# Performance work log

Measured on AMD Instinct MI355X. Metric: run time of the kernel, lower is better.

Reference implementation:

```python
import jax, jax.numpy as jnp
import numpy as np

N_NODES = 50000
N_EDGES = 800000
IN_F = 128
HEADS = 8
HEAD_DIM = 16
ALPHA = 0.2  # LeakyReLU negative slope
EPS = 1e-6


def setup_inputs() -> dict:
    key = jax.random.key(0)
    k1, k2, k3, k4 = jax.random.split(key, 4)
    x = jax.random.normal(k1, (N_NODES, IN_F), dtype=jnp.float32)
    edge_index = jax.random.randint(k2, (2, N_EDGES), 0, N_NODES, dtype=jnp.int32)
    std = 1.0 / np.sqrt(IN_F)
    W = jax.random.uniform(k3, (HEADS, IN_F, HEAD_DIM), minval=-std, maxval=std, dtype=jnp.float32)
    a = jax.random.uniform(k4, (HEADS, 2 * HEAD_DIM, 1), minval=-std, maxval=std, dtype=jnp.float32)
    bias = jnp.zeros((HEADS * HEAD_DIM,), dtype=jnp.float32)
    return {"x": x, "edge_index": edge_index, "W": W, "a": a, "bias": bias}


def reference(x, edge_index, W, a, bias):
    N = x.shape[0]
    src = edge_index[0]
    tgt = edge_index[1]
    # per-head linear transform: [N, H, D]
    h = jnp.einsum('nf,hfd->nhd', x, W)
    # split attention vector: a = [a_src; a_tgt], each [H, D]
    a_src = a[:, :HEAD_DIM, 0]
    a_tgt = a[:, HEAD_DIM:, 0]
    # node-level partial scores, then gather (equivalent to concat@a on edges)
    s_node_src = jnp.einsum('nhd,hd->nh', h, a_src)  # [N, H]
    s_node_tgt = jnp.einsum('nhd,hd->nh', h, a_tgt)  # [N, H]
    scores = s_node_src[src] + s_node_tgt[tgt]       # [E, H]
    scores = jnp.where(scores >= 0, scores, ALPHA * scores)  # LeakyReLU
    # edge softmax per target node, per head (global max subtract + clamp, as in source)
    max_per_head = jnp.max(scores, axis=0, keepdims=True)    # [1, H]
    exp_scores = jnp.exp(jnp.clip(scores - max_per_head, -20.0, 20.0))  # [E, H]
    denom = jax.ops.segment_sum(exp_scores, tgt, num_segments=N) + EPS  # [N, H]
    attn = exp_scores / denom[tgt]                                      # [E, H]
    # weighted scatter-add aggregation
    weighted = h[src] * attn[:, :, None]                                # [E, H, D]
    agg = jax.ops.segment_sum(weighted, tgt, num_segments=N)            # [N, H, D]
    out = agg.reshape(N, HEADS * HEAD_DIM) + bias
    return out
```

## Files before the change

### kernel.cpp

```cpp
#include <hip/hip_runtime.h>
#include <stdint.h>

#define N_NODES 50000
#define N_EDGES 800000
#define IN_F 128
#define HEADS 8
#define HEAD_DIM 16
#define ALPHA 0.2f
#define EPSV 1e-6f

#define NB 196
#define CAP 4800

typedef short short8 __attribute__((ext_vector_type(8)));
typedef float floatx4 __attribute__((ext_vector_type(4)));

__device__ __forceinline__ float bf2f(unsigned v) {
    return __uint_as_float(v << 16);
}
__device__ __forceinline__ float bflo(unsigned v) {
    return __uint_as_float(v << 16);
}
__device__ __forceinline__ float bfhi(unsigned v) {
    return __uint_as_float(v & 0xffff0000u);
}
__device__ __forceinline__ unsigned f2bf(float f) {
    unsigned u = __float_as_uint(f);
    return (u + 0x7fffu + ((u >> 16) & 1u)) >> 16;
}

__global__ __launch_bounds__(256) void k_wt(const float* __restrict__ W,
                                            ushort* __restrict__ WTb,
                                            int* __restrict__ gcnt) {
    int i = blockIdx.x * 256 + threadIdx.x;
    int c = i >> 7, f = i & 127;
    WTb[i] = (ushort)f2bf(W[(c >> 4) * 2048 + f * 16 + (c & 15)]);
    if (i < NB) gcnt[i] = 0;
}

__global__ __launch_bounds__(256) void k1_mfma(const float* __restrict__ x,
                                               const ushort* __restrict__ WTb,
                                               const float* __restrict__ a,
                                               ushort* __restrict__ hb,
                                               float* __restrict__ s_src,
                                               float* __restrict__ s_tgt) {
    int t = threadIdx.x;
    int wave = t >> 6, lane = t & 63;
    int quad = lane >> 4, col = lane & 15;
    int nb = blockIdx.x * 64 + wave * 16;

    int na = nb + col;
    int nac = na < N_NODES ? na : (N_NODES - 1);
    const float* xrow = x + (size_t)nac * 128 + quad * 8;

    floatx4 acc[8];
    floatx4 z = {0.f, 0.f, 0.f, 0.f};
#pragma unroll
    for (int ct = 0; ct < 8; ct++) acc[ct] = z;

#pragma unroll
    for (int kc = 0; kc < 4; kc++) {
        float4 f0 = *(const float4*)(xrow + kc * 32);
        float4 f1 = *(const float4*)(xrow + kc * 32 + 4);
        short8 af;
        af[0] = (short)f2bf(f0.x); af[1] = (short)f2bf(f0.y);
        af[2] = (short)f2bf(f0.z); af[3] = (short)f2bf(f0.w);
        af[4] = (short)f2bf(f1.x); af[5] = (short)f2bf(f1.y);
        af[6] = (short)f2bf(f1.z); af[7] = (short)f2bf(f1.w);
#pragma unroll
        for (int ct = 0; ct < 8; ct++) {
            const ushort* wrow = WTb + (size_t)(ct * 16 + col) * 128 + kc * 32 + quad * 8;
            short8 bf = *(const short8*)wrow;
            acc[ct] = __builtin_amdgcn_mfma_f32_16x16x32_bf16(af, bf, acc[ct], 0, 0, 0);
        }
    }

    float af_s[8], af_t[8];
#pragma unroll
    for (int ct = 0; ct < 8; ct++) {
        af_s[ct] = a[ct * 32 + col];
        af_t[ct] = a[ct * 32 + 16 + col];
    }

#pragma unroll
    for (int r = 0; r < 4; r++) {
        int node = nb + quad * 4 + r;
        bool nv = (node < N_NODES);
        if (nv) {
            ushort* hrow = hb + (size_t)node * 128 + col;
#pragma unroll
            for (int ct = 0; ct < 8; ct++)
                hrow[ct * 16] = (ushort)f2bf(acc[ct][r]);
        }
        float ps[8], pt[8];
#pragma unroll
        for (int ct = 0; ct < 8; ct++) {
            float hs = acc[ct][r];
            float vs = hs * af_s[ct];
            float vt = hs * af_t[ct];
#pragma unroll
            for (int off = 1; off < 16; off <<= 1) {
                vs += __shfl_xor(vs, off, 64);
                vt += __shfl_xor(vt, off, 64);
            }
            ps[ct] = vs; pt[ct] = vt;
        }
        if (nv && col == 0) {
            *(float4*)(s_src + (size_t)node * 8)     = make_float4(ps[0], ps[1], ps[2], ps[3]);
            *(float4*)(s_src + (size_t)node * 8 + 4) = make_float4(ps[4], ps[5], ps[6], ps[7]);
            *(float4*)(s_tgt + (size_t)node * 8)     = make_float4(pt[0], pt[1], pt[2], pt[3]);
            *(float4*)(s_tgt + (size_t)node * 8 + 4) = make_float4(pt[4], pt[5], pt[6], pt[7]);
        }
    }
}

__global__ __launch_bounds__(256) void k_passA(const int* __restrict__ srcA,
                                               const int* __restrict__ tgtA,
                                               int* __restrict__ gcnt,
                                               unsigned* __restrict__ bucketbuf) {
    __shared__ int lcnt[NB];
    __shared__ int lbase[NB];
    int t = threadIdx.x;
    if (t < NB) lcnt[t] = 0;
    __syncthreads();

    int base = blockIdx.x * 2048 + t;
    int tg[8], sr[8];
    bool vld[8];
#pragma unroll
    for (int k = 0; k < 8; k++) {
        int e = base + k * 256;
        vld[k] = (e < N_EDGES);
        int ee = vld[k] ? e : 0;
        tg[k] = tgtA[ee];
        sr[k] = srcA[ee];
    }
#pragma unroll
    for (int k = 0; k < 8; k++)
        if (vld[k]) atomicAdd(&lcnt[tg[k] >> 8], 1);
    __syncthreads();
    if (t < NB) {
        int c = lcnt[t];
        lbase[t] = (c > 0) ? atomicAdd(&gcnt[t], c) : 0;
        lcnt[t] = 0;
    }
    __syncthreads();
#pragma unroll
    for (int k = 0; k < 8; k++) {
        if (vld[k]) {
            int b = tg[k] >> 8;
            int off = atomicAdd(&lcnt[b], 1);
            int pos = lbase[b] + off;
            if (pos < CAP)
                bucketbuf[(size_t)b * CAP + pos] =
                    ((unsigned)(tg[k] & 255) << 16) | (unsigned)sr[k];
        }
    }
}

__global__ __launch_bounds__(256) void k_passB(const unsigned* __restrict__ bucketbuf,
                                               const int* __restrict__ gcnt,
                                               int* __restrict__ rowptr,
                                               ushort* __restrict__ src16) {
    __shared__ int bin[256];
    __shared__ int wsum[4];
    __shared__ int woff[4];
    __shared__ int sbase;
    __shared__ ushort stage[CAP];
    int t = threadIdx.x, lane = t & 63, w = t >> 6;
    int b = blockIdx.x;

    bin[t] = 0;
    int g = (t < NB) ? gcnt[t] : 0;
    int incg = g;
#pragma unroll
    for (int off = 1; off < 64; off <<= 1) {
        int nn = __shfl_up(incg, off, 64);
        if (lane >= off) incg += nn;
    }
    if (lane == 63) wsum[w] = incg;
    __syncthreads();
    if (t == 0) {
        woff[0] = 0;
        woff[1] = wsum[0];
        woff[2] = wsum[0] + wsum[1];
        woff[3] = wsum[0] + wsum[1] + wsum[2];
    }
    __syncthreads();
    if (t == b) sbase = woff[w] + incg - g;
    if (b == 0 && t == 0) rowptr[N_NODES] = N_EDGES;
    __syncthreads();
    int base = sbase;
    int n = gcnt[b]; if (n > CAP) n = CAP;
    const unsigned* buf = bucketbuf + (size_t)b * CAP;

    for (int i = t; i < n; i += 256)
        atomicAdd(&bin[buf[i] >> 16], 1);
    __syncthreads();
    int v = bin[t];
    int inc = v;
#pragma unroll
    for (int off = 1; off < 64; off <<= 1) {
        int nn = __shfl_up(inc, off, 64);
        if (lane >= off) inc += nn;
    }
    if (lane == 63) wsum[w] = inc;
    __syncthreads();
    if (t == 0) {
        woff[0] = 0;
        woff[1] = wsum[0];
        woff[2] = wsum[0] + wsum[1];
        woff[3] = wsum[0] + wsum[1] + wsum[2];
    }
    __syncthreads();
    int excl = woff[w] + inc - v;
    int node = b * 256 + t;
    if (node < N_NODES) rowptr[node] = base + excl;
    __syncthreads();
    bin[t] = excl;
    __syncthreads();
    for (int i = t; i < n; i += 256) {
        unsigned p = buf[i];
        int off = atomicAdd(&bin[p >> 16], 1);
        stage[off] = (ushort)(p & 0xffffu);
    }
    __syncthreads();
    for (int i = t; i < n; i += 256)
        src16[base + i] = stage[i];
}

__global__ __launch_bounds__(256) void k_fused(const int* __restrict__ rowptr,
                                               const ushort* __restrict__ src16,
                                               const float* __restrict__ s_src,
                                               const float* __restrict__ s_tgt,
                                               const unsigned* __restrict__ h16,
                                               const float* __restrict__ bias,
                                               float* __restrict__ outb) {
    int t = threadIdx.x;
    int wave = t >> 6, lane = t & 63;
    int half = lane >> 5, hl = lane & 31;
    int n = blockIdx.x * 8 + wave * 2 + half;
    int head = hl >> 2;
    int c = 4 * hl;

    const uint2* h2 = (const uint2*)h16;

    float st = s_tgt[n * 8 + head];
    int begin = rowptr[n], end = rowptr[n + 1];

    float ax = 0.f, ay = 0.f, az = 0.f, aw = 0.f, den = 0.f;
    int e = begin;
    for (; e + 3 < end; e += 4) {
        int s0 = src16[e];
        int s1 = src16[e + 1];
        int s2 = src16[e + 2];
        int s3 = src16[e + 3];
        float t0 = s_src[s0 * 8 + head];
        float t1 = s_src[s1 * 8 + head];
        float t2 = s_src[s2 * 8 + head];
        float t3 = s_src[s3 * 8 + head];
        uint2 p0 = h2[s0 * 32 + hl];
        uint2 p1 = h2[s1 * 32 + hl];
        uint2 p2 = h2[s2 * 32 + hl];
        uint2 p3 = h2[s3 * 32 + hl];
        float v0 = t0 + st; v0 = v0 >= 0.f ? v0 : ALPHA * v0;
        float v1 = t1 + st; v1 = v1 >= 0.f ? v1 : ALPHA * v1;
        float v2 = t2 + st; v2 = v2 >= 0.f ? v2 : ALPHA * v2;
        float v3 = t3 + st; v3 = v3 >= 0.f ? v3 : ALPHA * v3;
        float x0 = __expf(fminf(fmaxf(v0, -20.f), 20.f));
        float x1 = __expf(fminf(fmaxf(v1, -20.f), 20.f));
        float x2 = __expf(fminf(fmaxf(v2, -20.f), 20.f));
        float x3 = __expf(fminf(fmaxf(v3, -20.f), 20.f));
        den += (x0 + x1) + (x2 + x3);
        ax = fmaf(x0, bflo(p0.x), fmaf(x1, bflo(p1.x), fmaf(x2, bflo(p2.x), fmaf(x3, bflo(p3.x), ax))));
        ay = fmaf(x0, bfhi(p0.x), fmaf(x1, bfhi(p1.x), fmaf(x2, bfhi(p2.x), fmaf(x3, bfhi(p3.x), ay))));
        az = fmaf(x0, bflo(p0.y), fmaf(x1, bflo(p1.y), fmaf(x2, bflo(p2.y), fmaf(x3, bflo(p3.y), az))));
        aw = fmaf(x0, bfhi(p0.y), fmaf(x1, bfhi(p1.y), fmaf(x2, bfhi(p2.y), fmaf(x3, bfhi(p3.y), aw))));
    }
    for (; e < end; e++) {
        int sA = src16[e];
        float ssA = s_src[sA * 8 + head];
        uint2 pA = h2[sA * 32 + hl];
        float vA = ssA + st; vA = vA >= 0.f ? vA : ALPHA * vA;
        float exA = __expf(fminf(fmaxf(vA, -20.f), 20.f));
        den += exA;
        ax = fmaf(exA, bflo(pA.x), ax);
        ay = fmaf(exA, bfhi(pA.x), ay);
        az = fmaf(exA, bflo(pA.y), az);
        aw = fmaf(exA, bfhi(pA.y), aw);
    }
    float r = 1.f / (den + EPSV);
    float4 b = *(const float4*)(bias + c);
    float4 o;
    o.x = fmaf(ax, r, b.x);
    o.y = fmaf(ay, r, b.y);
    o.z = fmaf(az, r, b.z);
    o.w = fmaf(aw, r, b.w);
    *(float4*)(outb + (size_t)n * 128 + c) = o;
}

extern "C" void kernel_launch(void* const* d_in, const int* in_sizes, int n_in,
                              void* d_out, int out_size, void* d_ws, size_t ws_size,
                              hipStream_t stream) {
    const float* x    = (const float*)d_in[0];
    const int*   ei   = (const int*)d_in[1];
    const float* W    = (const float*)d_in[2];
    const float* a    = (const float*)d_in[3];
    const float* bias = (const float*)d_in[4];
    float* outb = (float*)d_out;

    char* ws = (char*)d_ws;
    ushort* hb        = (ushort*)(ws);
    float* s_src      = (float*)(ws + 12800000);
    float* s_tgt      = (float*)(ws + 14400000);
    int*   rowptr     = (int*)  (ws + 16000000);
    ushort* src16     = (ushort*)(ws + 16200064);
    int*   gcnt       = (int*)  (ws + 17800064);
    ushort* WTb       = (ushort*)(ws + 17902528);
    unsigned* bucketbuf = (unsigned*)(ws + 17935296);

    const int* srcA = ei;
    const int* tgtA = ei + N_EDGES;

    hipLaunchKernelGGL(k_wt,      dim3(64),    dim3(256), 0, stream, W, WTb, gcnt);
    hipLaunchKernelGGL(k1_mfma,   dim3(782),   dim3(256), 0, stream, x, WTb, a, hb, s_src, s_tgt);
    hipLaunchKernelGGL(k_passA,   dim3(391),   dim3(256), 0, stream, srcA, tgtA, gcnt, bucketbuf);
    hipLaunchKernelGGL(k_passB,   dim3(196),   dim3(256), 0, stream, bucketbuf, gcnt, rowptr, src16);
    hipLaunchKernelGGL(k_fused,   dim3(6250),  dim3(256), 0, stream, rowptr, src16, s_src, s_tgt, (const unsigned*)hb, bias, outb);
}
```

Measured before the change: 168.8 us.

## Merge node transform and edge bucketing into one launch; unroll aggregation by eight

The MFMA node-transform kernel and the edge-bucketing pass A become one kernel with interleaved block roles: every third block does bucketing and the other two do transform tiles. This removes one launch and lets the compute-bound and atomic-heavy work overlap on the GPU. Separately, the per-node aggregation loop is unrolled to eight edges per iteration, with a four-edge step before the scalar tail, so more gathers are in flight. Costs are higher register pressure in the fused kernel and in the unrolled loop, and the transform blocks now carry the bucketing code's LDS footprint.

```diff
diff --git a/kernel.cpp b/kernel.cpp
--- a/kernel.cpp
+++ b/kernel.cpp
@@ -15,9 +15,6 @@
 typedef short short8 __attribute__((ext_vector_type(8)));
 typedef float floatx4 __attribute__((ext_vector_type(4)));
 
-__device__ __forceinline__ float bf2f(unsigned v) {
-    return __uint_as_float(v << 16);
-}
 __device__ __forceinline__ float bflo(unsigned v) {
     return __uint_as_float(v << 16);
 }
@@ -38,16 +35,65 @@
     if (i < NB) gcnt[i] = 0;
 }
 
-__global__ __launch_bounds__(256) void k1_mfma(const float* __restrict__ x,
-                                               const ushort* __restrict__ WTb,
-                                               const float* __restrict__ a,
-                                               ushort* __restrict__ hb,
-                                               float* __restrict__ s_src,
-                                               float* __restrict__ s_tgt) {
+__global__ __launch_bounds__(256) void k_mid(const float* __restrict__ x,
+                                             const ushort* __restrict__ WTb,
+                                             const float* __restrict__ a,
+                                             ushort* __restrict__ hb,
+                                             float* __restrict__ s_src,
+                                             float* __restrict__ s_tgt,
+                                             const int* __restrict__ srcA,
+                                             const int* __restrict__ tgtA,
+                                             int* __restrict__ gcnt,
+                                             unsigned* __restrict__ bucketbuf) {
+    int bi = blockIdx.x;
+    int q3 = bi / 3, r3 = bi - q3 * 3;
     int t = threadIdx.x;
+
+    if (r3 == 2) {
+        __shared__ int lcnt[NB];
+        __shared__ int lbase[NB];
+        if (t < NB) lcnt[t] = 0;
+        __syncthreads();
+
+        int base = q3 * 2048 + t;
+        int tg[8], sr[8];
+        bool vld[8];
+#pragma unroll
+        for (int k = 0; k < 8; k++) {
+            int e = base + k * 256;
+            vld[k] = (e < N_EDGES);
+            int ee = vld[k] ? e : 0;
+            tg[k] = tgtA[ee];
+            sr[k] = srcA[ee];
+        }
+#pragma unroll
+        for (int k = 0; k < 8; k++)
+            if (vld[k]) atomicAdd(&lcnt[tg[k] >> 8], 1);
+        __syncthreads();
+        if (t < NB) {
+            int c = lcnt[t];
+            lbase[t] = (c > 0) ? atomicAdd(&gcnt[t], c) : 0;
+            lcnt[t] = 0;
+        }
+        __syncthreads();
+#pragma unroll
+        for (int k = 0; k < 8; k++) {
+            if (vld[k]) {
+                int b = tg[k] >> 8;
+                int off = atomicAdd(&lcnt[b], 1);
+                int pos = lbase[b] + off;
+                if (pos < CAP)
+                    bucketbuf[(size_t)b * CAP + pos] =
+                        ((unsigned)(tg[k] & 255) << 16) | (unsigned)sr[k];
+            }
+        }
+        return;
+    }
+
+    int mb = q3 * 2 + r3;
     int wave = t >> 6, lane = t & 63;
     int quad = lane >> 4, col = lane & 15;
-    int nb = blockIdx.x * 64 + wave * 16;
+    int nb = mb * 64 + wave * 16;
 
     int na = nb + col;
     int nac = na < N_NODES ? na : (N_NODES - 1);
@@ -110,50 +156,6 @@
             *(float4*)(s_src + (size_t)node * 8 + 4) = make_float4(ps[4], ps[5], ps[6], ps[7]);
             *(float4*)(s_tgt + (size_t)node * 8)     = make_float4(pt[0], pt[1], pt[2], pt[3]);
             *(float4*)(s_tgt + (size_t)node * 8 + 4) = make_float4(pt[4], pt[5], pt[6], pt[7]);
-        }
-    }
-}
-
-__global__ __launch_bounds__(256) void k_passA(const int* __restrict__ srcA,
-                                               const int* __restrict__ tgtA,
-                                               int* __restrict__ gcnt,
-                                               unsigned* __restrict__ bucketbuf) {
-    __shared__ int lcnt[NB];
-    __shared__ int lbase[NB];
-    int t = threadIdx.x;
-    if (t < NB) lcnt[t] = 0;
-    __syncthreads();
-
-    int base = blockIdx.x * 2048 + t;
-    int tg[8], sr[8];
-    bool vld[8];
-#pragma unroll
-    for (int k = 0; k < 8; k++) {
-        int e = base + k * 256;
-        vld[k] = (e < N_EDGES);
-        int ee = vld[k] ? e : 0;
-        tg[k] = tgtA[ee];
-        sr[k] = srcA[ee];
-    }
-#pragma unroll
-    for (int k = 0; k < 8; k++)
-        if (vld[k]) atomicAdd(&lcnt[tg[k] >> 8], 1);
-    __syncthreads();
-    if (t < NB) {
-        int c = lcnt[t];
-        lbase[t] = (c > 0) ? atomicAdd(&gcnt[t], c) : 0;
-        lcnt[t] = 0;
-    }
-    __syncthreads();
-#pragma unroll
-    for (int k = 0; k < 8; k++) {
-        if (vld[k]) {
-            int b = tg[k] >> 8;
-            int off = atomicAdd(&lcnt[b], 1);
-            int pos = lbase[b] + off;
-            if (pos < CAP)
-                bucketbuf[(size_t)b * CAP + pos] =
-                    ((unsigned)(tg[k] & 255) << 16) | (unsigned)sr[k];
         }
     }
 }
@@ -250,7 +252,58 @@
 
     float ax = 0.f, ay = 0.f, az = 0.f, aw = 0.f, den = 0.f;
     int e = begin;
-    for (; e + 3 < end; e += 4) {
+    for (; e + 7 < end; e += 8) {
+        int s0 = src16[e];
+        int s1 = src16[e + 1];
+        int s2 = src16[e + 2];
+        int s3 = src16[e + 3];
+        int s4 = src16[e + 4];
+        int s5 = src16[e + 5];
+        int s6 = src16[e + 6];
+        int s7 = src16[e + 7];
+        float t0 = s_src[s0 * 8 + head];
+        float t1 = s_src[s1 * 8 + head];
+        float t2 = s_src[s2 * 8 + head];
+        float t3 = s_src[s3 * 8 + head];
+        float t4 = s_src[s4 * 8 + head];
+        float t5 = s_src[s5 * 8 + head];
+        float t6 = s_src[s6 * 8 + head];
+        float t7 = s_src[s7 * 8 + head];
+        uint2 p0 = h2[s0 * 32 + hl];
+        uint2 p1 = h2[s1 * 32 + hl];
+        uint2 p2 = h2[s2 * 32 + hl];
+        uint2 p3 = h2[s3 * 32 + hl];
+        uint2 p4 = h2[s4 * 32 + hl];
+        uint2 p5 = h2[s5 * 32 + hl];
+        uint2 p6 = h2[s6 * 32 + hl];
+        uint2 p7 = h2[s7 * 32 + hl];
+        float v0 = t0 + st; v0 = v0 >= 0.f ? v0 : ALPHA * v0;
+        float v1 = t1 + st; v1 = v1 >= 0.f ? v1 : ALPHA * v1;
+        float v2 = t2 + st; v2 = v2 >= 0.f ? v2 : ALPHA * v2;
+        float v3 = t3 + st; v3 = v3 >= 0.f ? v3 : ALPHA * v3;
+        float v4 = t4 + st; v4 = v4 >= 0.f ? v4 : ALPHA * v4;
+        float v5 = t5 + st; v5 = v5 >= 0.f ? v5 : ALPHA * v5;
+        float v6 = t6 + st; v6 = v6 >= 0.f ? v6 : ALPHA * v6;
+        float v7 = t7 + st; v7 = v7 >= 0.f ? v7 : ALPHA * v7;
+        float x0 = __expf(fminf(fmaxf(v0, -20.f), 20.f));
+        float x1 = __expf(fminf(fmaxf(v1, -20.f), 20.f));
+        float x2 = __expf(fminf(fmaxf(v2, -20.f), 20.f));
+        float x3 = __expf(fminf(fmaxf(v3, -20.f), 20.f));
+        float x4 = __expf(fminf(fmaxf(v4, -20.f), 20.f));
+        float x5 = __expf(fminf(fmaxf(v5, -20.f), 20.f));
+        float x6 = __expf(fminf(fmaxf(v6, -20.f), 20.f));
+        float x7 = __expf(fminf(fmaxf(v7, -20.f), 20.f));
+        den += ((x0 + x1) + (x2 + x3)) + ((x4 + x5) + (x6 + x7));
+        ax = fmaf(x0, bflo(p0.x), fmaf(x1, bflo(p1.x), fmaf(x2, bflo(p2.x), fmaf(x3, bflo(p3.x), ax))));
+        ax = fmaf(x4, bflo(p4.x), fmaf(x5, bflo(p5.x), fmaf(x6, bflo(p6.x), fmaf(x7, bflo(p7.x), ax))));
+        ay = fmaf(x0, bfhi(p0.x), fmaf(x1, bfhi(p1.x), fmaf(x2, bfhi(p2.x), fmaf(x3, bfhi(p3.x), ay))));
+        ay = fmaf(x4, bfhi(p4.x), fmaf(x5, bfhi(p5.x), fmaf(x6, bfhi(p6.x), fmaf(x7, bfhi(p7.x), ay))));
+        az = fmaf(x0, bflo(p0.y), fmaf(x1, bflo(p1.y), fmaf(x2, bflo(p2.y), fmaf(x3, bflo(p3.y), az))));
+        az = fmaf(x4, bflo(p4.y), fmaf(x5, bflo(p5.y), fmaf(x6, bflo(p6.y), fmaf(x7, bflo(p7.y), az))));
+        aw = fmaf(x0, bfhi(p0.y), fmaf(x1, bfhi(p1.y), fmaf(x2, bfhi(p2.y), fmaf(x3, bfhi(p3.y), aw))));
+        aw = fmaf(x4, bfhi(p4.y), fmaf(x5, bfhi(p5.y), fmaf(x6, bfhi(p6.y), fmaf(x7, bfhi(p7.y), aw))));
+    }
+    if (e + 3 < end) {
         int s0 = src16[e];
         int s1 = src16[e + 1];
         int s2 = src16[e + 2];
@@ -276,6 +329,7 @@
         ay = fmaf(x0, bfhi(p0.x), fmaf(x1, bfhi(p1.x), fmaf(x2, bfhi(p2.x), fmaf(x3, bfhi(p3.x), ay))));
         az = fmaf(x0, bflo(p0.y), fmaf(x1, bflo(p1.y), fmaf(x2, bflo(p2.y), fmaf(x3, bflo(p3.y), az))));
         aw = fmaf(x0, bfhi(p0.y), fmaf(x1, bfhi(p1.y), fmaf(x2, bfhi(p2.y), fmaf(x3, bfhi(p3.y), aw))));
+        e += 4;
     }
     for (; e < end; e++) {
         int sA = src16[e];
@@ -322,9 +376,9 @@
     const int* srcA = ei;
     const int* tgtA = ei + N_EDGES;
 
-    hipLaunchKernelGGL(k_wt,      dim3(64),    dim3(256), 0, stream, W, WTb, gcnt);
-    hipLaunchKernelGGL(k1_mfma,   dim3(782),   dim3(256), 0, stream, x, WTb, a, hb, s_src, s_tgt);
-    hipLaunchKernelGGL(k_passA,   dim3(391),   dim3(256), 0, stream, srcA, tgtA, gcnt, bucketbuf);
-    hipLaunchKernelGGL(k_passB,   dim3(196),   dim3(256), 0, stream, bucketbuf, gcnt, rowptr, src16);
-    hipLaunchKernelGGL(k_fused,   dim3(6250),  dim3(256), 0, stream, rowptr, src16, s_src, s_tgt, (const unsigned*)hb, bias, outb);
-}
+    hipLaunchKernelGGL(k_wt,    dim3(64),   dim3(256), 0, stream, W, WTb, gcnt);
+    hipLaunchKernelGGL(k_mid,   dim3(1173), dim3(256), 0, stream,
+                       x, WTb, a, hb, s_src, s_tgt, srcA, tgtA, gcnt, bucketbuf);
+    hipLaunchKernelGGL(k_passB, dim3(196),  dim3(256), 0, stream, bucketbuf, gcnt, rowptr, src16);
+    hipLaunchKernelGGL(k_fused, dim3(6250), dim3(256), 0, stream, rowptr, src16, s_src, s_tgt, (const unsigned*)hb, bias, outb);
+}
```

Result: faster. 156.6 us (-7.2%).
